# Kernel optimization log

Hardware: AMD Instinct MI355X
Metric: run time of the kernel (lower is better)

Reference implementation:

```python
import jax, jax.numpy as jnp
import numpy as np

N = 1048576          # total octree nodes across the batch
C = 64               # in_channels
BATCH_SIZE = 16
GROUP = 16           # clamped: min_group_channels(4)*group(32) > 64 -> group = 64//4
CPG = C // GROUP     # channels_per_group = 4
EPS = 1e-5


def setup_inputs() -> dict:
    key = jax.random.key(0)
    k1, k2, k3, k4 = jax.random.split(key, 4)
    data = jax.random.normal(k1, (N, C), dtype=jnp.float32)
    batch_id = jnp.sort(jax.random.randint(k2, (N,), 0, BATCH_SIZE)).astype(jnp.int32)
    weights = jax.random.normal(k3, (1, C), dtype=jnp.float32)
    bias = jax.random.normal(k4, (1, C), dtype=jnp.float32)
    return {"data": data, "batch_id": batch_id, "weights": weights, "bias": bias}


def _adjust_for_group(t):
    # sum over channels within each group, broadcast back to all channels
    if CPG > 1:
        t = t.reshape(-1, GROUP, CPG).sum(-1, keepdims=True)
        t = jnp.broadcast_to(t, (t.shape[0], GROUP, CPG)).reshape(-1, C)
    return t


def reference(data, batch_id, weights, bias):
    # per-sample element counts, scaled so the group-sum of means is a true group mean
    ones = jnp.ones((data.shape[0],), dtype=data.dtype)
    count = jax.ops.segment_sum(ones, batch_id, num_segments=BATCH_SIZE)[:, None]  # [B,1]
    count = count * CPG
    inv_count = 1.0 / (count + EPS)

    mean = jax.ops.segment_sum(data, batch_id, num_segments=BATCH_SIZE) * inv_count  # [B,C]
    mean = _adjust_for_group(mean)
    out = data - mean[batch_id]  # gather broadcast [N,C]

    var = jax.ops.segment_sum(out * out, batch_id, num_segments=BATCH_SIZE) * inv_count
    var = _adjust_for_group(var)
    inv_std = jax.lax.rsqrt(var + EPS)

    out = out * inv_std[batch_id]
    return out * weights + bias
```

## Files before the change

kernel.cpp:

```cpp
#include <hip/hip_runtime.h>

#define NBATCH 16
#define NCH 64
#define CPG 4
#define NGRP 16
#define EPSV 1e-5f


__global__ void ogn_stats(const float* __restrict__ data,
                          const int* __restrict__ bid,
                          float* __restrict__ S1,
                          float* __restrict__ S2,
                          int* __restrict__ cnt,
                          int N, int rows_per_block) {
    __shared__ float ls1[NBATCH * NCH];
    __shared__ float ls2[NBATCH * NCH];
    __shared__ int   lcnt[NBATCH];

    for (int i = threadIdx.x; i < NBATCH * NCH; i += blockDim.x) {
        ls1[i] = 0.f;
        ls2[i] = 0.f;
    }
    if (threadIdx.x < NBATCH) lcnt[threadIdx.x] = 0;
    __syncthreads();

    const int t     = threadIdx.x;
    const int c4    = t & 15;
    const int rlane = t >> 4;

    long long row_begin = (long long)blockIdx.x * rows_per_block;
    long long row_end   = row_begin + rows_per_block;
    if (row_end > N) row_end = N;

    const float4* data4 = (const float4*)data;

    float4 s1 = make_float4(0.f, 0.f, 0.f, 0.f);
    float4 s2 = make_float4(0.f, 0.f, 0.f, 0.f);
    int cur = -1;
    int c   = 0;

    for (long long r = row_begin + rlane; r < row_end; r += 16) {
        int b = bid[r];
        if (b != cur) {
            if (cur >= 0) {
                int base = cur * NCH + c4 * 4;
                atomicAdd(&ls1[base + 0], s1.x);
                atomicAdd(&ls1[base + 1], s1.y);
                atomicAdd(&ls1[base + 2], s1.z);
                atomicAdd(&ls1[base + 3], s1.w);
                atomicAdd(&ls2[base + 0], s2.x);
                atomicAdd(&ls2[base + 1], s2.y);
                atomicAdd(&ls2[base + 2], s2.z);
                atomicAdd(&ls2[base + 3], s2.w);
                if (c4 == 0) atomicAdd(&lcnt[cur], c);
            }
            s1 = make_float4(0.f, 0.f, 0.f, 0.f);
            s2 = make_float4(0.f, 0.f, 0.f, 0.f);
            c = 0;
            cur = b;
        }
        float4 v = data4[r * 16 + c4];
        s1.x += v.x; s1.y += v.y; s1.z += v.z; s1.w += v.w;
        s2.x += v.x * v.x; s2.y += v.y * v.y; s2.z += v.z * v.z; s2.w += v.w * v.w;
        c++;
    }
    if (cur >= 0) {
        int base = cur * NCH + c4 * 4;
        atomicAdd(&ls1[base + 0], s1.x);
        atomicAdd(&ls1[base + 1], s1.y);
        atomicAdd(&ls1[base + 2], s1.z);
        atomicAdd(&ls1[base + 3], s1.w);
        atomicAdd(&ls2[base + 0], s2.x);
        atomicAdd(&ls2[base + 1], s2.y);
        atomicAdd(&ls2[base + 2], s2.z);
        atomicAdd(&ls2[base + 3], s2.w);
        if (c4 == 0) atomicAdd(&lcnt[cur], c);
    }
    __syncthreads();

    for (int i = threadIdx.x; i < NBATCH * NCH; i += blockDim.x) {
        float v1 = ls1[i];
        float v2 = ls2[i];
        if (v1 != 0.f) atomicAdd(&S1[i], v1);
        if (v2 != 0.f) atomicAdd(&S2[i], v2);
    }
    if (threadIdx.x < NBATCH) {
        int v = lcnt[threadIdx.x];
        if (v != 0) atomicAdd(&cnt[threadIdx.x], v);
    }
}

__global__ void ogn_params(const float* __restrict__ S1,
                           const float* __restrict__ S2,
                           const int* __restrict__ cnt,
                           const float* __restrict__ w,
                           const float* __restrict__ bias,
                           float* __restrict__ A,
                           float* __restrict__ B) {
    int t = threadIdx.x;
    if (t >= NBATCH * NGRP) return;
    int b = t >> 4;
    int g = t & 15;

    int base = b * NCH + g * CPG;
    float s1g = 0.f, s2g = 0.f;
#pragma unroll
    for (int k = 0; k < CPG; ++k) {
        s1g += S1[base + k];
        s2g += S2[base + k];
    }
    float countf    = (float)cnt[b] * (float)CPG;
    float inv_count = 1.f / (countf + EPSV);
    float mean      = s1g * inv_count;
    float var       = inv_count * (s2g - 2.f * mean * s1g + countf * mean * mean);
    float inv_std   = rsqrtf(var + EPSV);

#pragma unroll
    for (int k = 0; k < CPG; ++k) {
        int ch = g * CPG + k;
        float wv = w[ch];
        float bv = bias[ch];
        A[b * NCH + ch] = inv_std * wv;
        B[b * NCH + ch] = bv - mean * inv_std * wv;
    }
}

__global__ void ogn_apply(const float* __restrict__ data,
                          const int* __restrict__ bid,
                          const float* __restrict__ A,
                          const float* __restrict__ B,
                          float* __restrict__ out,
                          long long total4) {
    const float4* d4 = (const float4*)data;
    const float4* A4 = (const float4*)A;
    const float4* B4 = (const float4*)B;
    float4* o4 = (float4*)out;

    long long i      = (long long)blockIdx.x * blockDim.x + threadIdx.x;
    long long stride = (long long)gridDim.x * blockDim.x;

    for (; i < total4; i += stride) {
        long long row = i >> 4;
        int c4 = (int)(i & 15);
        int b  = bid[row];
        float4 v  = d4[i];
        float4 a  = A4[b * 16 + c4];
        float4 bb = B4[b * 16 + c4];
        float4 r;
        r.x = fmaf(v.x, a.x, bb.x);
        r.y = fmaf(v.y, a.y, bb.y);
        r.z = fmaf(v.z, a.z, bb.z);
        r.w = fmaf(v.w, a.w, bb.w);
        o4[i] = r;
    }
}

extern "C" void kernel_launch(void* const* d_in, const int* in_sizes, int n_in,
                              void* d_out, int out_size, void* d_ws, size_t ws_size,
                              hipStream_t stream) {
    const float* data = (const float*)d_in[0];
    const int*   bid  = (const int*)d_in[1];
    const float* w    = (const float*)d_in[2];
    const float* bias = (const float*)d_in[3];
    float* out = (float*)d_out;

    int N = in_sizes[1];

    char* ws = (char*)d_ws;
    float* S1  = (float*)(ws + 0);
    float* S2  = (float*)(ws + 4096);
    int*   cnt = (int*)  (ws + 8192);
    float* A   = (float*)(ws + 8448);
    float* B   = (float*)(ws + 12544);

    hipMemsetAsync(d_ws, 0, 8256, stream);

    const int NB1 = 1024;
    int rows_per_block = (N + NB1 - 1) / NB1;
    ogn_stats<<<NB1, 256, 0, stream>>>(data, bid, S1, S2, cnt, N, rows_per_block);

    ogn_params<<<1, 256, 0, stream>>>(S1, S2, cnt, w, bias, A, B);

    long long total4 = (long long)N * (NCH / 4);
    int NB3 = 8192;
    ogn_apply<<<NB3, 256, 0, stream>>>(data, bid, A, B, out, total4);
}
```

Before: 515.3 us.

## Fuse param kernel into apply, unroll stats loop, retune grid sizes

Removes the single-block params kernel. Each apply block now recomputes the per-batch scale and shift from the global sums into shared memory, which eliminates one launch and its serialization. The stats loop is unrolled by four with a fast path for rows that share a batch id, so more loads are in flight. The stats grid is doubled and the apply grid halved. Every apply block redundantly reads the sums and computes rsqrt, and the wider stats grid adds more global atomics.

```diff
diff --git a/kernel.cpp b/kernel.cpp
--- a/kernel.cpp
+++ b/kernel.cpp
@@ -39,43 +39,64 @@
     int cur = -1;
     int c   = 0;
 
-    for (long long r = row_begin + rlane; r < row_end; r += 16) {
+#define FLUSH() do { if (cur >= 0) {                                   \
+        int base_ = cur * NCH + c4 * 4;                                \
+        atomicAdd(&ls1[base_ + 0], s1.x);                              \
+        atomicAdd(&ls1[base_ + 1], s1.y);                              \
+        atomicAdd(&ls1[base_ + 2], s1.z);                              \
+        atomicAdd(&ls1[base_ + 3], s1.w);                              \
+        atomicAdd(&ls2[base_ + 0], s2.x);                              \
+        atomicAdd(&ls2[base_ + 1], s2.y);                              \
+        atomicAdd(&ls2[base_ + 2], s2.z);                              \
+        atomicAdd(&ls2[base_ + 3], s2.w);                              \
+        if (c4 == 0) atomicAdd(&lcnt[cur], c);                         \
+    } } while (0)
+
+#define ACCV(vv) do {                                                  \
+        s1.x += (vv).x; s1.y += (vv).y; s1.z += (vv).z; s1.w += (vv).w;\
+        s2.x = fmaf((vv).x, (vv).x, s2.x);                             \
+        s2.y = fmaf((vv).y, (vv).y, s2.y);                             \
+        s2.z = fmaf((vv).z, (vv).z, s2.z);                             \
+        s2.w = fmaf((vv).w, (vv).w, s2.w);                             \
+    } while (0)
+
+#define ACC1(bb, vv) do {                                              \
+        if ((bb) != cur) {                                             \
+            FLUSH();                                                   \
+            s1 = make_float4(0.f, 0.f, 0.f, 0.f);                      \
+            s2 = make_float4(0.f, 0.f, 0.f, 0.f);                      \
+            c = 0; cur = (bb);                                         \
+        }                                                              \
+        ACCV(vv); c++;                                                 \
+    } while (0)
+
+    long long r = row_begin + rlane;
+
+    for (; r + 48 < row_end; r += 64) {
+        int b0 = bid[r];
+        int b1 = bid[r + 16];
+        int b2 = bid[r + 32];
+        int b3 = bid[r + 48];
+        float4 v0 = data4[r * 16 + c4];
+        float4 v1 = data4[(r + 16) * 16 + c4];
+        float4 v2 = data4[(r + 32) * 16 + c4];
+        float4 v3 = data4[(r + 48) * 16 + c4];
+        if (((b0 == cur) & (b1 == cur) & (b2 == cur) & (b3 == cur)) != 0) {
+            ACCV(v0); ACCV(v1); ACCV(v2); ACCV(v3);
+            c += 4;
+        } else {
+            ACC1(b0, v0);
+            ACC1(b1, v1);
+            ACC1(b2, v2);
+            ACC1(b3, v3);
+        }
+    }
+    for (; r < row_end; r += 16) {
         int b = bid[r];
-        if (b != cur) {
-            if (cur >= 0) {
-                int base = cur * NCH + c4 * 4;
-                atomicAdd(&ls1[base + 0], s1.x);
-                atomicAdd(&ls1[base + 1], s1.y);
-                atomicAdd(&ls1[base + 2], s1.z);
-                atomicAdd(&ls1[base + 3], s1.w);
-                atomicAdd(&ls2[base + 0], s2.x);
-                atomicAdd(&ls2[base + 1], s2.y);
-                atomicAdd(&ls2[base + 2], s2.z);
-                atomicAdd(&ls2[base + 3], s2.w);
-                if (c4 == 0) atomicAdd(&lcnt[cur], c);
-            }
-            s1 = make_float4(0.f, 0.f, 0.f, 0.f);
-            s2 = make_float4(0.f, 0.f, 0.f, 0.f);
-            c = 0;
-            cur = b;
-        }
         float4 v = data4[r * 16 + c4];
-        s1.x += v.x; s1.y += v.y; s1.z += v.z; s1.w += v.w;
-        s2.x += v.x * v.x; s2.y += v.y * v.y; s2.z += v.z * v.z; s2.w += v.w * v.w;
-        c++;
-    }
-    if (cur >= 0) {
-        int base = cur * NCH + c4 * 4;
-        atomicAdd(&ls1[base + 0], s1.x);
-        atomicAdd(&ls1[base + 1], s1.y);
-        atomicAdd(&ls1[base + 2], s1.z);
-        atomicAdd(&ls1[base + 3], s1.w);
-        atomicAdd(&ls2[base + 0], s2.x);
-        atomicAdd(&ls2[base + 1], s2.y);
-        atomicAdd(&ls2[base + 2], s2.z);
-        atomicAdd(&ls2[base + 3], s2.w);
-        if (c4 == 0) atomicAdd(&lcnt[cur], c);
-    }
+        ACC1(b, v);
+    }
+    FLUSH();
     __syncthreads();
 
     for (int i = threadIdx.x; i < NBATCH * NCH; i += blockDim.x) {
@@ -88,52 +109,54 @@
         int v = lcnt[threadIdx.x];
         if (v != 0) atomicAdd(&cnt[threadIdx.x], v);
     }
-}
-
-__global__ void ogn_params(const float* __restrict__ S1,
-                           const float* __restrict__ S2,
-                           const int* __restrict__ cnt,
-                           const float* __restrict__ w,
-                           const float* __restrict__ bias,
-                           float* __restrict__ A,
-                           float* __restrict__ B) {
-    int t = threadIdx.x;
-    if (t >= NBATCH * NGRP) return;
-    int b = t >> 4;
-    int g = t & 15;
-
-    int base = b * NCH + g * CPG;
-    float s1g = 0.f, s2g = 0.f;
-#pragma unroll
-    for (int k = 0; k < CPG; ++k) {
-        s1g += S1[base + k];
-        s2g += S2[base + k];
-    }
-    float countf    = (float)cnt[b] * (float)CPG;
-    float inv_count = 1.f / (countf + EPSV);
-    float mean      = s1g * inv_count;
-    float var       = inv_count * (s2g - 2.f * mean * s1g + countf * mean * mean);
-    float inv_std   = rsqrtf(var + EPSV);
-
-#pragma unroll
-    for (int k = 0; k < CPG; ++k) {
-        int ch = g * CPG + k;
-        float wv = w[ch];
-        float bv = bias[ch];
-        A[b * NCH + ch] = inv_std * wv;
-        B[b * NCH + ch] = bv - mean * inv_std * wv;
-    }
+
+#undef ACC1
+#undef ACCV
+#undef FLUSH
 }
 
 __global__ void ogn_apply(const float* __restrict__ data,
                           const int* __restrict__ bid,
-                          const float* __restrict__ A,
-                          const float* __restrict__ B,
+                          const float* __restrict__ S1,
+                          const float* __restrict__ S2,
+                          const int* __restrict__ cnt,
+                          const float* __restrict__ w,
+                          const float* __restrict__ bias,
                           float* __restrict__ out,
                           long long total4) {
+    __shared__ float4 lA[NBATCH * NGRP];
+    __shared__ float4 lB[NBATCH * NGRP];
+
+    const int t = threadIdx.x;
+    if (t < NBATCH * NGRP) {
+        int b = t >> 4;
+        int g = t & 15;
+        int base = b * NCH + g * CPG;
+        float s1g = 0.f, s2g = 0.f;
+#pragma unroll
+        for (int k = 0; k < CPG; ++k) {
+            s1g += S1[base + k];
+            s2g += S2[base + k];
+        }
+        float countf    = (float)cnt[b] * (float)CPG;
+        float inv_count = 1.f / (countf + EPSV);
+        float mean      = s1g * inv_count;
+        float var       = inv_count * (s2g - 2.f * mean * s1g + countf * mean * mean);
+        float inv_std   = rsqrtf(var + EPSV);
+
+        float4 wv = ((const float4*)w)[g];
+        float4 bv = ((const float4*)bias)[g];
+        float4 a4, b4;
+        a4.x = inv_std * wv.x; b4.x = bv.x - mean * a4.x;
+        a4.y = inv_std * wv.y; b4.y = bv.y - mean * a4.y;
+        a4.z = inv_std * wv.z; b4.z = bv.z - mean * a4.z;
+        a4.w = inv_std * wv.w; b4.w = bv.w - mean * a4.w;
+        lA[b * NGRP + g] = a4;
+        lB[b * NGRP + g] = b4;
+    }
+    __syncthreads();
+
     const float4* d4 = (const float4*)data;
-    const float4* A4 = (const float4*)A;
-    const float4* B4 = (const float4*)B;
     float4* o4 = (float4*)out;
 
     long long i      = (long long)blockIdx.x * blockDim.x + threadIdx.x;
@@ -144,8 +167,8 @@
         int c4 = (int)(i & 15);
         int b  = bid[row];
         float4 v  = d4[i];
-        float4 a  = A4[b * 16 + c4];
-        float4 bb = B4[b * 16 + c4];
+        float4 a  = lA[b * NGRP + c4];
+        float4 bb = lB[b * NGRP + c4];
         float4 r;
         r.x = fmaf(v.x, a.x, bb.x);
         r.y = fmaf(v.y, a.y, bb.y);
@@ -170,18 +193,14 @@
     float* S1  = (float*)(ws + 0);
     float* S2  = (float*)(ws + 4096);
     int*   cnt = (int*)  (ws + 8192);
-    float* A   = (float*)(ws + 8448);
-    float* B   = (float*)(ws + 12544);
 
     hipMemsetAsync(d_ws, 0, 8256, stream);
 
-    const int NB1 = 1024;
+    const int NB1 = 2048;
     int rows_per_block = (N + NB1 - 1) / NB1;
     ogn_stats<<<NB1, 256, 0, stream>>>(data, bid, S1, S2, cnt, N, rows_per_block);
 
-    ogn_params<<<1, 256, 0, stream>>>(S1, S2, cnt, w, bias, A, B);
-
     long long total4 = (long long)N * (NCH / 4);
-    int NB3 = 8192;
-    ogn_apply<<<NB3, 256, 0, stream>>>(data, bid, A, B, out, total4);
+    const int NB3 = 4096;
+    ogn_apply<<<NB3, 256, 0, stream>>>(data, bid, S1, S2, cnt, w, bias, out, total4);
 }
```

Result: no change. 512.0 us (-0.6%).

## Fuse params into apply kernel, add uniform-batch fast paths and nontemporal stores

Applied to the files above, without the earlier changes.

Removes the single-block params kernel by having every apply block compute the per-batch scale and shift into shared memory. Both the stats and apply kernels now use contiguous row ranges per block, with a fast path for ranges that hold a single batch id: the per-row id load is skipped, the loop is unrolled by four, and output is written with nontemporal stores. The stats grid is raised to 2048 blocks. Each apply block now repeats the small params computation, and any range that spans a batch boundary still takes the general per-row path.

```diff
diff --git a/kernel.cpp b/kernel.cpp
--- a/kernel.cpp
+++ b/kernel.cpp
@@ -6,13 +6,16 @@
 #define NGRP 16
 #define EPSV 1e-5f
 
-
-__global__ void ogn_stats(const float* __restrict__ data,
-                          const int* __restrict__ bid,
-                          float* __restrict__ S1,
-                          float* __restrict__ S2,
-                          int* __restrict__ cnt,
-                          int N, int rows_per_block) {
+typedef float f32x4 __attribute__((ext_vector_type(4)));
+
+
+__global__ __launch_bounds__(256)
+void ogn_stats(const float* __restrict__ data,
+               const int* __restrict__ bid,
+               float* __restrict__ S1,
+               float* __restrict__ S2,
+               int* __restrict__ cnt,
+               int N, int rows_per_block) {
     __shared__ float ls1[NBATCH * NCH];
     __shared__ float ls2[NBATCH * NCH];
     __shared__ int   lcnt[NBATCH];
@@ -30,18 +33,77 @@
 
     long long row_begin = (long long)blockIdx.x * rows_per_block;
     long long row_end   = row_begin + rows_per_block;
+    if (row_begin > N) row_begin = N;
     if (row_end > N) row_end = N;
 
     const float4* data4 = (const float4*)data;
 
-    float4 s1 = make_float4(0.f, 0.f, 0.f, 0.f);
-    float4 s2 = make_float4(0.f, 0.f, 0.f, 0.f);
-    int cur = -1;
-    int c   = 0;
-
-    for (long long r = row_begin + rlane; r < row_end; r += 16) {
-        int b = bid[r];
-        if (b != cur) {
+#define ACCV(vv) do {                                                  \
+        s1.x += (vv).x; s1.y += (vv).y; s1.z += (vv).z; s1.w += (vv).w;\
+        s2.x = fmaf((vv).x, (vv).x, s2.x);                             \
+        s2.y = fmaf((vv).y, (vv).y, s2.y);                             \
+        s2.z = fmaf((vv).z, (vv).z, s2.z);                             \
+        s2.w = fmaf((vv).w, (vv).w, s2.w);                             \
+    } while (0)
+
+    if (row_begin < row_end) {
+        const int b0 = bid[row_begin];
+        const int b1 = bid[row_end - 1];
+
+        if (b0 == b1) {
+            float4 s1 = make_float4(0.f, 0.f, 0.f, 0.f);
+            float4 s2 = make_float4(0.f, 0.f, 0.f, 0.f);
+            long long r = row_begin + rlane;
+            for (; r + 48 < row_end; r += 64) {
+                float4 v0 = data4[r * 16 + c4];
+                float4 v1 = data4[(r + 16) * 16 + c4];
+                float4 v2 = data4[(r + 32) * 16 + c4];
+                float4 v3 = data4[(r + 48) * 16 + c4];
+                ACCV(v0); ACCV(v1); ACCV(v2); ACCV(v3);
+            }
+            for (; r < row_end; r += 16) {
+                float4 v = data4[r * 16 + c4];
+                ACCV(v);
+            }
+            int base = b0 * NCH + c4 * 4;
+            atomicAdd(&ls1[base + 0], s1.x);
+            atomicAdd(&ls1[base + 1], s1.y);
+            atomicAdd(&ls1[base + 2], s1.z);
+            atomicAdd(&ls1[base + 3], s1.w);
+            atomicAdd(&ls2[base + 0], s2.x);
+            atomicAdd(&ls2[base + 1], s2.y);
+            atomicAdd(&ls2[base + 2], s2.z);
+            atomicAdd(&ls2[base + 3], s2.w);
+            if (t == 0) lcnt[b0] = (int)(row_end - row_begin);
+        } else {
+            float4 s1 = make_float4(0.f, 0.f, 0.f, 0.f);
+            float4 s2 = make_float4(0.f, 0.f, 0.f, 0.f);
+            int cur = -1;
+            int c   = 0;
+            for (long long r = row_begin + rlane; r < row_end; r += 16) {
+                int b = bid[r];
+                if (b != cur) {
+                    if (cur >= 0) {
+                        int base = cur * NCH + c4 * 4;
+                        atomicAdd(&ls1[base + 0], s1.x);
+                        atomicAdd(&ls1[base + 1], s1.y);
+                        atomicAdd(&ls1[base + 2], s1.z);
+                        atomicAdd(&ls1[base + 3], s1.w);
+                        atomicAdd(&ls2[base + 0], s2.x);
+                        atomicAdd(&ls2[base + 1], s2.y);
+                        atomicAdd(&ls2[base + 2], s2.z);
+                        atomicAdd(&ls2[base + 3], s2.w);
+                        if (c4 == 0) atomicAdd(&lcnt[cur], c);
+                    }
+                    s1 = make_float4(0.f, 0.f, 0.f, 0.f);
+                    s2 = make_float4(0.f, 0.f, 0.f, 0.f);
+                    c = 0;
+                    cur = b;
+                }
+                float4 v = data4[r * 16 + c4];
+                ACCV(v);
+                c++;
+            }
             if (cur >= 0) {
                 int base = cur * NCH + c4 * 4;
                 atomicAdd(&ls1[base + 0], s1.x);
@@ -54,28 +116,9 @@
                 atomicAdd(&ls2[base + 3], s2.w);
                 if (c4 == 0) atomicAdd(&lcnt[cur], c);
             }
-            s1 = make_float4(0.f, 0.f, 0.f, 0.f);
-            s2 = make_float4(0.f, 0.f, 0.f, 0.f);
-            c = 0;
-            cur = b;
-        }
-        float4 v = data4[r * 16 + c4];
-        s1.x += v.x; s1.y += v.y; s1.z += v.z; s1.w += v.w;
-        s2.x += v.x * v.x; s2.y += v.y * v.y; s2.z += v.z * v.z; s2.w += v.w * v.w;
-        c++;
-    }
-    if (cur >= 0) {
-        int base = cur * NCH + c4 * 4;
-        atomicAdd(&ls1[base + 0], s1.x);
-        atomicAdd(&ls1[base + 1], s1.y);
-        atomicAdd(&ls1[base + 2], s1.z);
-        atomicAdd(&ls1[base + 3], s1.w);
-        atomicAdd(&ls2[base + 0], s2.x);
-        atomicAdd(&ls2[base + 1], s2.y);
-        atomicAdd(&ls2[base + 2], s2.z);
-        atomicAdd(&ls2[base + 3], s2.w);
-        if (c4 == 0) atomicAdd(&lcnt[cur], c);
-    }
+        }
+    }
+#undef ACCV
     __syncthreads();
 
     for (int i = threadIdx.x; i < NBATCH * NCH; i += blockDim.x) {
@@ -90,69 +133,107 @@
     }
 }
 
-__global__ void ogn_params(const float* __restrict__ S1,
-                           const float* __restrict__ S2,
-                           const int* __restrict__ cnt,
-                           const float* __restrict__ w,
-                           const float* __restrict__ bias,
-                           float* __restrict__ A,
-                           float* __restrict__ B) {
-    int t = threadIdx.x;
-    if (t >= NBATCH * NGRP) return;
-    int b = t >> 4;
-    int g = t & 15;
-
-    int base = b * NCH + g * CPG;
-    float s1g = 0.f, s2g = 0.f;
+__global__ __launch_bounds__(256)
+void ogn_apply(const float* __restrict__ data,
+               const int* __restrict__ bid,
+               const float* __restrict__ S1,
+               const float* __restrict__ S2,
+               const int* __restrict__ cnt,
+               const float* __restrict__ w,
+               const float* __restrict__ bias,
+               float* __restrict__ out,
+               int N, int rows_per_block) {
+    __shared__ float4 lA[NBATCH * NGRP];
+    __shared__ float4 lB[NBATCH * NGRP];
+
+    const int t = threadIdx.x;
+    if (t < NBATCH * NGRP) {
+        int b = t >> 4;
+        int g = t & 15;
+        int base = b * NCH + g * CPG;
+        float s1g = 0.f, s2g = 0.f;
 #pragma unroll
-    for (int k = 0; k < CPG; ++k) {
-        s1g += S1[base + k];
-        s2g += S2[base + k];
-    }
-    float countf    = (float)cnt[b] * (float)CPG;
-    float inv_count = 1.f / (countf + EPSV);
-    float mean      = s1g * inv_count;
-    float var       = inv_count * (s2g - 2.f * mean * s1g + countf * mean * mean);
-    float inv_std   = rsqrtf(var + EPSV);
-
-#pragma unroll
-    for (int k = 0; k < CPG; ++k) {
-        int ch = g * CPG + k;
-        float wv = w[ch];
-        float bv = bias[ch];
-        A[b * NCH + ch] = inv_std * wv;
-        B[b * NCH + ch] = bv - mean * inv_std * wv;
-    }
-}
-
-__global__ void ogn_apply(const float* __restrict__ data,
-                          const int* __restrict__ bid,
-                          const float* __restrict__ A,
-                          const float* __restrict__ B,
-                          float* __restrict__ out,
-                          long long total4) {
+        for (int k = 0; k < CPG; ++k) {
+            s1g += S1[base + k];
+            s2g += S2[base + k];
+        }
+        float countf    = (float)cnt[b] * (float)CPG;
+        float inv_count = 1.f / (countf + EPSV);
+        float mean      = s1g * inv_count;
+        float var       = inv_count * (s2g - 2.f * mean * s1g + countf * mean * mean);
+        float inv_std   = rsqrtf(var + EPSV);
+
+        float4 wv = ((const float4*)w)[g];
+        float4 bv = ((const float4*)bias)[g];
+        float4 a4, b4;
+        a4.x = inv_std * wv.x; b4.x = bv.x - mean * a4.x;
+        a4.y = inv_std * wv.y; b4.y = bv.y - mean * a4.y;
+        a4.z = inv_std * wv.z; b4.z = bv.z - mean * a4.z;
+        a4.w = inv_std * wv.w; b4.w = bv.w - mean * a4.w;
+        lA[b * NGRP + g] = a4;
+        lB[b * NGRP + g] = b4;
+    }
+    __syncthreads();
+
+    const int c4    = t & 15;
+    const int rlane = t >> 4;
+
+    long long row_begin = (long long)blockIdx.x * rows_per_block;
+    long long row_end   = row_begin + rows_per_block;
+    if (row_begin > N) row_begin = N;
+    if (row_end > N) row_end = N;
+    if (row_begin >= row_end) return;
+
     const float4* d4 = (const float4*)data;
-    const float4* A4 = (const float4*)A;
-    const float4* B4 = (const float4*)B;
     float4* o4 = (float4*)out;
 
-    long long i      = (long long)blockIdx.x * blockDim.x + threadIdx.x;
-    long long stride = (long long)gridDim.x * blockDim.x;
-
-    for (; i < total4; i += stride) {
-        long long row = i >> 4;
-        int c4 = (int)(i & 15);
-        int b  = bid[row];
-        float4 v  = d4[i];
-        float4 a  = A4[b * 16 + c4];
-        float4 bb = B4[b * 16 + c4];
-        float4 r;
-        r.x = fmaf(v.x, a.x, bb.x);
-        r.y = fmaf(v.y, a.y, bb.y);
-        r.z = fmaf(v.z, a.z, bb.z);
-        r.w = fmaf(v.w, a.w, bb.w);
-        o4[i] = r;
-    }
+    const int b0 = bid[row_begin];
+    const int b1 = bid[row_end - 1];
+
+#define FMA4(res_, vv, a_, b_) do {                                    \
+        (res_).x = fmaf((vv).x, (a_).x, (b_).x);                       \
+        (res_).y = fmaf((vv).y, (a_).y, (b_).y);                       \
+        (res_).z = fmaf((vv).z, (a_).z, (b_).z);                       \
+        (res_).w = fmaf((vv).w, (a_).w, (b_).w);                       \
+    } while (0)
+
+    if (b0 == b1) {
+        const float4 a  = lA[b0 * NGRP + c4];
+        const float4 bb = lB[b0 * NGRP + c4];
+        long long r = row_begin + rlane;
+        for (; r + 48 < row_end; r += 64) {
+            float4 v0 = d4[r * 16 + c4];
+            float4 v1 = d4[(r + 16) * 16 + c4];
+            float4 v2 = d4[(r + 32) * 16 + c4];
+            float4 v3 = d4[(r + 48) * 16 + c4];
+            f32x4 r0, r1, r2, r3;
+            FMA4(r0, v0, a, bb);
+            FMA4(r1, v1, a, bb);
+            FMA4(r2, v2, a, bb);
+            FMA4(r3, v3, a, bb);
+            __builtin_nontemporal_store(r0, (f32x4*)&o4[r * 16 + c4]);
+            __builtin_nontemporal_store(r1, (f32x4*)&o4[(r + 16) * 16 + c4]);
+            __builtin_nontemporal_store(r2, (f32x4*)&o4[(r + 32) * 16 + c4]);
+            __builtin_nontemporal_store(r3, (f32x4*)&o4[(r + 48) * 16 + c4]);
+        }
+        for (; r < row_end; r += 16) {
+            float4 v = d4[r * 16 + c4];
+            f32x4 res;
+            FMA4(res, v, a, bb);
+            __builtin_nontemporal_store(res, (f32x4*)&o4[r * 16 + c4]);
+        }
+    } else {
+        for (long long r = row_begin + rlane; r < row_end; r += 16) {
+            int b = bid[r];
+            float4 v  = d4[r * 16 + c4];
+            float4 a  = lA[b * NGRP + c4];
+            float4 bb = lB[b * NGRP + c4];
+            f32x4 res;
+            FMA4(res, v, a, bb);
+            __builtin_nontemporal_store(res, (f32x4*)&o4[r * 16 + c4]);
+        }
+    }
+#undef FMA4
 }
 
 extern "C" void kernel_launch(void* const* d_in, const int* in_sizes, int n_in,
@@ -170,18 +251,13 @@
     float* S1  = (float*)(ws + 0);
     float* S2  = (float*)(ws + 4096);
     int*   cnt = (int*)  (ws + 8192);
-    float* A   = (float*)(ws + 8448);
-    float* B   = (float*)(ws + 12544);
 
     hipMemsetAsync(d_ws, 0, 8256, stream);
 
-    const int NB1 = 1024;
-    int rows_per_block = (N + NB1 - 1) / NB1;
-    ogn_stats<<<NB1, 256, 0, stream>>>(data, bid, S1, S2, cnt, N, rows_per_block);
-
-    ogn_params<<<1, 256, 0, stream>>>(S1, S2, cnt, w, bias, A, B);
-
-    long long total4 = (long long)N * (NCH / 4);
-    int NB3 = 8192;
-    ogn_apply<<<NB3, 256, 0, stream>>>(data, bid, A, B, out, total4);
+    const int NB = 2048;
+    int rows_per_block = (int)(((long long)N + NB - 1) / NB);
+
+    ogn_stats<<<NB, 256, 0, stream>>>(data, bid, S1, S2, cnt, N, rows_per_block);
+    ogn_apply<<<NB, 256, 0, stream>>>(data, bid, S1, S2, cnt, w, bias, out,
+                                      N, rows_per_block);
 }
```

After: 505.2 us. No clear change (-2.0%).
